# Optimization experiments

Hardware: AMD Instinct MI355X
Metric: run time of the kernel (lower is better)

Reference implementation:

```python
import jax, jax.numpy as jnp
import numpy as np

D_MODEL = 384
N_LAYER = 4
VOCAB = 5000
D_INNER = 768   # 2 * d_model (mamba expand=2)
D_STATE = 16
DT_RANK = 24    # ceil(d_model/16)
D_CONV = 4
EPS = 1e-5
BATCH = 4
SEQ = 2048


def setup_inputs():
    key = jax.random.key(0)
    ks = jax.random.split(key, 12)
    tokens = jax.random.randint(ks[0], (BATCH, SEQ), 0, VOCAB)
    embed = jax.random.normal(ks[1], (VOCAB, D_MODEL), jnp.float32) * 0.02
    norm_w = jnp.ones((N_LAYER, D_MODEL), jnp.float32)
    in_proj_w = jax.random.normal(ks[2], (N_LAYER, 2 * D_INNER, D_MODEL), jnp.float32) * 0.02
    conv_w = jax.random.normal(ks[3], (N_LAYER, D_INNER, D_CONV), jnp.float32) * 0.2
    conv_b = jnp.zeros((N_LAYER, D_INNER), jnp.float32)
    x_proj_w = jax.random.normal(ks[4], (N_LAYER, DT_RANK + 2 * D_STATE, D_INNER), jnp.float32) * 0.05
    dt_proj_w = jax.random.normal(ks[5], (N_LAYER, D_INNER, DT_RANK), jnp.float32) * 0.05
    # bias ~ inverse-softplus of small dt init (dt ~ [0.001, 0.1])
    dt_proj_b = -4.0 + jax.random.normal(ks[6], (N_LAYER, D_INNER), jnp.float32) * 0.5
    # S4D-real init: A = -[1..d_state]
    A_log = jnp.log(jnp.broadcast_to(jnp.arange(1, D_STATE + 1, dtype=jnp.float32), (N_LAYER, D_INNER, D_STATE)))
    D_param = jnp.ones((N_LAYER, D_INNER), jnp.float32)
    out_proj_w = jax.random.normal(ks[7], (N_LAYER, D_MODEL, D_INNER), jnp.float32) * 0.02
    final_norm_w = jnp.ones((D_MODEL,), jnp.float32)
    return {"tokens": tokens, "embed": embed, "norm_w": norm_w, "in_proj_w": in_proj_w,
            "conv_w": conv_w, "conv_b": conv_b, "x_proj_w": x_proj_w, "dt_proj_w": dt_proj_w,
            "dt_proj_b": dt_proj_b, "A_log": A_log, "D_param": D_param,
            "out_proj_w": out_proj_w, "final_norm_w": final_norm_w}


def rmsnorm(x, w):
    return x * w * jax.lax.rsqrt(jnp.mean(x * x, axis=-1, keepdims=True) + EPS)


def mamba_mixer(x, in_w, cw, cb, xpw, dtw, dtb, A_log, Dp, ow):
    B, L, _ = x.shape
    xz = jnp.einsum('bld,ed->ble', x, in_w)          # (B,L,2E)
    xin, z = jnp.split(xz, 2, axis=-1)               # (B,L,E) each
    # causal depthwise conv1d (kernel 4, left-pad 3)
    xc = jnp.swapaxes(xin, 1, 2)                     # (B,E,L)
    xc = jax.lax.conv_general_dilated(
        xc, cw[:, None, :], (1,), [(D_CONV - 1, 0)],
        dimension_numbers=('NCH', 'OIH', 'NCH'), feature_group_count=D_INNER)
    xin = jax.nn.silu(jnp.swapaxes(xc, 1, 2) + cb)   # (B,L,E)
    proj = jnp.einsum('ble,re->blr', xin, xpw)       # (B,L,dtR+2N)
    dt, Bs, Cs = jnp.split(proj, [DT_RANK, DT_RANK + D_STATE], axis=-1)
    dt = jax.nn.softplus(jnp.einsum('blr,er->ble', dt, dtw) + dtb)  # (B,L,E)
    A = -jnp.exp(A_log)                               # (E,N)

    def step(h, inp):
        dt_t, B_t, C_t, x_t = inp                     # (B,E),(B,N),(B,N),(B,E)
        h = h * jnp.exp(dt_t[..., None] * A) + (dt_t * x_t)[..., None] * B_t[:, None, :]
        y = jnp.einsum('ben,bn->be', h, C_t)
        return h, y

    h0 = jnp.zeros((B, D_INNER, D_STATE), x.dtype)
    _, ys = jax.lax.scan(step, h0, (jnp.swapaxes(dt, 0, 1), jnp.swapaxes(Bs, 0, 1),
                                    jnp.swapaxes(Cs, 0, 1), jnp.swapaxes(xin, 0, 1)))
    y = jnp.swapaxes(ys, 0, 1) + xin * Dp             # skip via D
    y = y * jax.nn.silu(z)                            # gate
    return jnp.einsum('ble,de->bld', y, ow)


def reference(tokens, embed, norm_w, in_proj_w, conv_w, conv_b, x_proj_w,
              dt_proj_w, dt_proj_b, A_log, D_param, out_proj_w, final_norm_w):
    x = embed[tokens]                                 # (B,L,D)
    for i in range(N_LAYER):
        x = x + mamba_mixer(rmsnorm(x, norm_w[i]), in_proj_w[i], conv_w[i], conv_b[i],
                            x_proj_w[i], dt_proj_w[i], dt_proj_b[i], A_log[i],
                            D_param[i], out_proj_w[i])
    x = rmsnorm(x, final_norm_w)
    return jnp.einsum('bld,vd->blv', x, embed)        # tied lm_head -> logits
```

## Files before the change

### kernel.cpp

```cpp
#include <hip/hip_runtime.h>
#include <hip/hip_bf16.h>

#define D_MODEL 384
#define N_LAYER 4
#define VOCAB   5000
#define D_INNER 768
#define D_STATE 16
#define DT_RANK 24
#define D_CONV  4
#define BATCH   4
#define SEQ     2048
#define ROWS    (BATCH*SEQ)
#define NCHUNK  64
#define CLEN    32

typedef __attribute__((ext_vector_type(8))) short bf16x8;
typedef __attribute__((ext_vector_type(4))) float f32x4;

static __device__ __forceinline__ ushort f2b(float f) {
    uint u = __float_as_uint(f);
    return (ushort)((u + 0x7FFFu + ((u >> 16) & 1u)) >> 16);
}
static __device__ __forceinline__ float b2f(ushort u) {
    return __uint_as_float((uint)u << 16);
}
static __device__ __forceinline__ float softplus_f(float v) {
    return fmaxf(v, 0.f) + __logf(1.f + __expf(-fabsf(v)));
}

static __device__ __forceinline__ void gl_lds16(const void* g, void* l) {
    __builtin_amdgcn_global_load_lds(
        (const __attribute__((address_space(1))) void*)g,
        (__attribute__((address_space(3))) void*)l, 16, 0, 0);
}

template<int N> static __device__ __forceinline__ void waitcnt_vm() {
    __builtin_amdgcn_s_waitcnt((N & 0xF) | (7 << 4) | (0xF << 8) | (((N >> 4) & 3) << 14));
}

__global__ __launch_bounds__(256)
void prep_k(const float* __restrict__ inw, const float* __restrict__ outw,
            const float* __restrict__ emb, const float* __restrict__ xpw,
            const float* __restrict__ dtw, const int* __restrict__ tokens,
            ushort* __restrict__ inw_b, ushort* __restrict__ outw_b,
            ushort* __restrict__ emb_b, ushort* __restrict__ wf,
            float* __restrict__ x)
{
    int idx = blockIdx.x * 256 + threadIdx.x;
    if (idx < 589824) {
        float4 v = reinterpret_cast<const float4*>(inw)[idx];
        ushort4 o; o.x=f2b(v.x); o.y=f2b(v.y); o.z=f2b(v.z); o.w=f2b(v.w);
        reinterpret_cast<ushort4*>(inw_b)[idx] = o;
    } else if (idx < 884736) {
        int i = idx - 589824;
        float4 v = reinterpret_cast<const float4*>(outw)[i];
        ushort4 o; o.x=f2b(v.x); o.y=f2b(v.y); o.z=f2b(v.z); o.w=f2b(v.w);
        reinterpret_cast<ushort4*>(outw_b)[i] = o;
    } else if (idx < 1364736) {
        int i = idx - 884736;
        float4 v = reinterpret_cast<const float4*>(emb)[i];
        ushort4 o; o.x=f2b(v.x); o.y=f2b(v.y); o.z=f2b(v.z); o.w=f2b(v.w);
        reinterpret_cast<ushort4*>(emb_b)[i] = o;
    } else if (idx < 4117248) {
        int i = idx - 1364736;
        int l = i / (896*768); int rk = i % (896*768);
        int r = rk / 768, k = rk % 768;
        float v = 0.f;
        if (r < 768) {
            const float* dr = dtw + ((size_t)l*768 + r)*24;
            const float* xc = xpw + (size_t)l*56*768 + k;
            #pragma unroll
            for (int q = 0; q < 24; ++q) v += dr[q] * xc[(size_t)q*768];
        } else if (r < 800) {
            v = xpw[((size_t)l*56 + 24 + (r-768))*768 + k];
        }
        wf[i] = f2b(v);
    } else {
        int i = idx - 4117248;
        int row = i / 96, c4 = i % 96;
        int tok = tokens[row];
        reinterpret_cast<float4*>(x)[(size_t)row * 96 + c4] =
            reinterpret_cast<const float4*>(emb)[(size_t)tok * 96 + c4];
    }
}

__global__ __launch_bounds__(256)
void rmsnorm_k(const float* __restrict__ xin, const float* __restrict__ w,
               ushort* __restrict__ xout)
{
    int row  = blockIdx.x * 4 + (threadIdx.x >> 6);
    int lane = threadIdx.x & 63;
    const float* xr = xin + (size_t)row * D_MODEL;
    float v[6]; float ss = 0.f;
    #pragma unroll
    for (int j = 0; j < 6; ++j) { v[j] = xr[lane + 64*j]; ss += v[j]*v[j]; }
    #pragma unroll
    for (int m = 32; m; m >>= 1) ss += __shfl_xor(ss, m, 64);
    float r = rsqrtf(ss * (1.f/D_MODEL) + 1e-5f);
    ushort* yo = xout + (size_t)row * D_MODEL;
    #pragma unroll
    for (int j = 0; j < 6; ++j) yo[lane + 64*j] = f2b(v[j] * w[lane + 64*j] * r);
}

__global__ __launch_bounds__(256)
void conv_silu_k(const ushort* __restrict__ xz_b, const float* __restrict__ cw,
                 const float* __restrict__ cb, ushort* __restrict__ xout_b)
{
    int idx = blockIdx.x * 256 + threadIdx.x;
    int e4  = idx % 192;
    int row = idx / 192;
    int e   = e4 * 4;
    int l   = row & (SEQ - 1);

    float4 w0 = reinterpret_cast<const float4*>(cw)[e4*4 + 0];
    float4 w1 = reinterpret_cast<const float4*>(cw)[e4*4 + 1];
    float4 w2 = reinterpret_cast<const float4*>(cw)[e4*4 + 2];
    float4 w3 = reinterpret_cast<const float4*>(cw)[e4*4 + 3];
    float4 bv = reinterpret_cast<const float4*>(cb)[e4];
    float ac0 = bv.x, ac1 = bv.y, ac2 = bv.z, ac3 = bv.w;

    #pragma unroll
    for (int j = 0; j < 4; ++j) {
        if (l - j >= 0) {
            ushort4 v = *reinterpret_cast<const ushort4*>(
                &xz_b[(size_t)(row - j) * (2*D_INNER) + e]);
            float wj0 = (&w0.x)[3-j], wj1 = (&w1.x)[3-j],
                  wj2 = (&w2.x)[3-j], wj3 = (&w3.x)[3-j];
            ac0 += wj0 * b2f(v.x); ac1 += wj1 * b2f(v.y);
            ac2 += wj2 * b2f(v.z); ac3 += wj3 * b2f(v.w);
        }
    }
    ushort4 o;
    o.x = f2b(ac0 / (1.f + __expf(-ac0)));
    o.y = f2b(ac1 / (1.f + __expf(-ac1)));
    o.z = f2b(ac2 / (1.f + __expf(-ac2)));
    o.w = f2b(ac3 / (1.f + __expf(-ac3)));
    *reinterpret_cast<ushort4*>(&xout_b[(size_t)row * D_INNER + e]) = o;
}

template<int TM, int TN, int EPI>
__global__ __launch_bounds__(256)
void gemm_lds(const ushort* __restrict__ A, int lda,
              const ushort* __restrict__ B, int ldb,
              float* __restrict__ C, int ldc,
              ushort* __restrict__ Cb, const float* __restrict__ bias,
              int N, int K)
{
    constexpr int FM = TM / 32, FN = TN / 32;
    constexpr int LPT = TM/64 + TN/64;
    __shared__ alignas(16) ushort As[3][TM * 32];
    __shared__ alignas(16) ushort Bs[3][TN * 32];
    int tid = threadIdx.x, w = tid >> 6, l = tid & 63;
    int wr = w >> 1, wc = w & 1;
    int row0 = blockIdx.y * TM, col0 = blockIdx.x * TN;
    int l15 = l & 15, g = l >> 4;
    int sr = l >> 2, sp = l & 3;

    f32x4 acc[FM][FN] = {};

    auto stage = [&](int buf, int k0) {
        #pragma unroll
        for (int j = 0; j < TM/64; ++j) {
            int ai = w * (TM/64) + j;
            int r  = ai * 16 + sr;
            int s  = sp ^ ((r >> 1) & 3);
            gl_lds16(&A[(size_t)(row0 + r) * lda + k0 + s*8], &As[buf][ai * 512]);
        }
        #pragma unroll
        for (int j = 0; j < TN/64; ++j) {
            int bi = w * (TN/64) + j;
            int r  = bi * 16 + sr;
            int s  = sp ^ ((r >> 1) & 3);
            gl_lds16(&B[(size_t)(col0 + r) * ldb + k0 + s*8], &Bs[buf][bi * 512]);
        }
    };

    int nk = K >> 5;
    stage(0, 0);
    if (nk > 1) stage(1, 32);

    int cur = 0, sbuf = 2;
    for (int t = 0; t < nk; ++t) {
        if (t < nk - 1) waitcnt_vm<LPT>();
        else            waitcnt_vm<0>();
        __builtin_amdgcn_sched_barrier(0);
        __builtin_amdgcn_s_barrier();
        __builtin_amdgcn_sched_barrier(0);
        if (t + 2 < nk) stage(sbuf, (t + 2) << 5);
        __builtin_amdgcn_sched_barrier(0);

        bf16x8 af[FM], bfr[FN];
        #pragma unroll
        for (int i = 0; i < FM; ++i) {
            int r = wr * (TM/2) + i*16 + l15;
            int p = g ^ ((r >> 1) & 3);
            af[i] = *reinterpret_cast<const bf16x8*>(&As[cur][r*32 + p*8]);
        }
        #pragma unroll
        for (int i = 0; i < FN; ++i) {
            int r = wc * (TN/2) + i*16 + l15;
            int p = g ^ ((r >> 1) & 3);
            bfr[i] = *reinterpret_cast<const bf16x8*>(&Bs[cur][r*32 + p*8]);
        }
        #pragma unroll
        for (int i = 0; i < FM; ++i)
            #pragma unroll
            for (int jj = 0; jj < FN; ++jj)
                acc[i][jj] = __builtin_amdgcn_mfma_f32_16x16x32_bf16(bfr[jj], af[i], acc[i][jj], 0, 0, 0);

        cur  = (cur  == 2) ? 0 : cur + 1;
        sbuf = (sbuf == 2) ? 0 : sbuf + 1;
    }

    #pragma unroll
    for (int i = 0; i < FM; ++i) {
        int m = row0 + wr * (TM/2) + i*16 + l15;
        #pragma unroll
        for (int jj = 0; jj < FN; ++jj) {
            int n0 = col0 + wc * (TN/2) + jj*16 + g*4;
            if (n0 < N) {
                f32x4 v = acc[i][jj];
                if (EPI == 2) {
                    float4* p = reinterpret_cast<float4*>(&C[(size_t)m * ldc + n0]);
                    float4 o = *p;
                    o.x += v[0]; o.y += v[1]; o.z += v[2]; o.w += v[3];
                    *p = o;
                } else if (EPI == 4) {
                    ushort4 o;
                    o.x = f2b(v[0]); o.y = f2b(v[1]); o.z = f2b(v[2]); o.w = f2b(v[3]);
                    *reinterpret_cast<ushort4*>(&Cb[(size_t)m * ldc + n0]) = o;
                } else if (EPI == 5) {
                    if (n0 < 768) {
                        float4 bv = *reinterpret_cast<const float4*>(&bias[n0]);
                        ushort4 o;
                        o.x = f2b(softplus_f(v[0] + bv.x));
                        o.y = f2b(softplus_f(v[1] + bv.y));
                        o.z = f2b(softplus_f(v[2] + bv.z));
                        o.w = f2b(softplus_f(v[3] + bv.w));
                        *reinterpret_cast<ushort4*>(&Cb[(size_t)m * ldc + n0]) = o;
                    } else {
                        float4 o; o.x = v[0]; o.y = v[1]; o.z = v[2]; o.w = v[3];
                        *reinterpret_cast<float4*>(&C[(size_t)m * 32 + (n0 - 768)]) = o;
                    }
                } else {
                    float4 o; o.x = v[0]; o.y = v[1]; o.z = v[2]; o.w = v[3];
                    *reinterpret_cast<float4*>(&C[(size_t)m * ldc + n0]) = o;
                }
            }
        }
    }
}


__global__ __launch_bounds__(256)
void scan_p1(const ushort* __restrict__ dtb, const ushort* __restrict__ xin_b,
             const float* __restrict__ bc, const float* __restrict__ A_log,
             ushort* __restrict__ h_end, ushort* __restrict__ decay)
{
    __shared__ float Bs[CLEN][16];
    int b = blockIdx.z, c = blockIdx.y;
    int e = blockIdx.x * 256 + threadIdx.x;
    size_t r0 = (size_t)b * SEQ + (size_t)c * CLEN;

    for (int i = threadIdx.x; i < CLEN*16; i += 256) {
        int l = i >> 4, n = i & 15;
        Bs[l][n] = bc[(r0 + l) * 32 + n];
    }
    __syncthreads();

    float a[16];
    const float4* ap = reinterpret_cast<const float4*>(A_log + e * D_STATE);
    #pragma unroll
    for (int q = 0; q < 4; ++q) {
        float4 av = ap[q];
        a[q*4+0] = -__expf(av.x); a[q*4+1] = -__expf(av.y);
        a[q*4+2] = -__expf(av.z); a[q*4+3] = -__expf(av.w);
    }

    const ushort* pdt = dtb   + r0 * D_INNER + e;
    const ushort* px  = xin_b + r0 * D_INNER + e;
    float h[16];
    #pragma unroll
    for (int n = 0; n < 16; ++n) h[n] = 0.f;
    float S = 0.f;
    float dtv = b2f(pdt[0]), xv = b2f(px[0]);

    for (int l = 0; l < CLEN; ++l) {
        float dtn = 0.f, xn2 = 0.f;
        if (l + 1 < CLEN) {
            dtn = b2f(pdt[(size_t)(l+1) * D_INNER]);
            xn2 = b2f(px [(size_t)(l+1) * D_INNER]);
        }
        float dtx = dtv * xv;
        S += dtv;
        const float4* br = reinterpret_cast<const float4*>(&Bs[l][0]);
        float4 B0 = br[0], B1 = br[1], B2 = br[2], B3 = br[3];
        float Bv[16] = {B0.x,B0.y,B0.z,B0.w, B1.x,B1.y,B1.z,B1.w,
                        B2.x,B2.y,B2.z,B2.w, B3.x,B3.y,B3.z,B3.w};
        #pragma unroll
        for (int n = 0; n < 16; ++n) {
            float ex = __expf(dtv * a[n]);
            h[n] = h[n] * ex + dtx * Bv[n];
        }
        dtv = dtn; xv = xn2;
    }

    size_t base = (((size_t)b * D_INNER + e) * D_STATE) * NCHUNK + c;
    #pragma unroll
    for (int n = 0; n < 16; ++n) {
        h_end[base + (size_t)n * NCHUNK] = f2b(h[n]);
        decay[base + (size_t)n * NCHUNK] = f2b(__expf(a[n] * S));
    }
}

__global__ __launch_bounds__(256)
void scan_p2(const ushort* __restrict__ h_end, const ushort* __restrict__ decay,
             ushort* __restrict__ h_init)
{
    int wid  = (blockIdx.x * 256 + threadIdx.x) >> 6;
    int lane = threadIdx.x & 63;
    size_t base = (size_t)wid * NCHUNK;
    float d = b2f(decay[base + lane]);
    float v = b2f(h_end[base + lane]);
    #pragma unroll
    for (int off = 1; off < 64; off <<= 1) {
        float dp = __shfl_up(d, off, 64);
        float vp = __shfl_up(v, off, 64);
        if (lane >= off) { v = fmaf(d, vp, v); d *= dp; }
    }
    float hi = __shfl_up(v, 1, 64);
    if (lane == 0) hi = 0.f;
    h_init[base + lane] = f2b(hi);
}

__global__ __launch_bounds__(256)
void scan_p3(const ushort* __restrict__ dtb, const ushort* __restrict__ xin_b,
             const ushort* __restrict__ xz_b, const float* __restrict__ bc,
             const float* __restrict__ A_log, const float* __restrict__ Dp,
             const ushort* __restrict__ h_init, ushort* __restrict__ y)
{
    __shared__ float BCs[CLEN][32];
    int b = blockIdx.z, c = blockIdx.y;
    int e = blockIdx.x * 256 + threadIdx.x;
    size_t r0 = (size_t)b * SEQ + (size_t)c * CLEN;

    for (int i = threadIdx.x; i < CLEN*32; i += 256) {
        int l = i >> 5, r = i & 31;
        BCs[l][r] = bc[(r0 + l) * 32 + r];
    }
    __syncthreads();

    float a[16];
    const float4* ap = reinterpret_cast<const float4*>(A_log + e * D_STATE);
    #pragma unroll
    for (int q = 0; q < 4; ++q) {
        float4 av = ap[q];
        a[q*4+0] = -__expf(av.x); a[q*4+1] = -__expf(av.y);
        a[q*4+2] = -__expf(av.z); a[q*4+3] = -__expf(av.w);
    }
    float dskip = Dp[e];

    float h[16];
    size_t hbase = (((size_t)b * D_INNER + e) * D_STATE) * NCHUNK + c;
    #pragma unroll
    for (int n = 0; n < 16; ++n) h[n] = b2f(h_init[hbase + (size_t)n * NCHUNK]);

    const ushort* pdt = dtb   + r0 * D_INNER + e;
    const ushort* px  = xin_b + r0 * D_INNER + e;
    const ushort* pz  = xz_b  + r0 * (2*D_INNER) + D_INNER + e;
    ushort*       py  = y     + r0 * D_INNER + e;

    float dtv = b2f(pdt[0]), xv = b2f(px[0]), zv = b2f(pz[0]);

    for (int l = 0; l < CLEN; ++l) {
        float dtn = 0.f, xn2 = 0.f, zn = 0.f;
        if (l + 1 < CLEN) {
            dtn = b2f(pdt[(size_t)(l+1) * D_INNER]);
            xn2 = b2f(px [(size_t)(l+1) * D_INNER]);
            zn  = b2f(pz [(size_t)(l+1) * (2*D_INNER)]);
        }
        float dtx = dtv * xv;
        const float4* br = reinterpret_cast<const float4*>(&BCs[l][0]);
        float4 B0 = br[0], B1 = br[1], B2 = br[2], B3 = br[3];
        float Bv[16] = {B0.x,B0.y,B0.z,B0.w, B1.x,B1.y,B1.z,B1.w,
                        B2.x,B2.y,B2.z,B2.w, B3.x,B3.y,B3.z,B3.w};
        #pragma unroll
        for (int n = 0; n < 16; ++n) {
            float ex = __expf(dtv * a[n]);
            h[n] = h[n] * ex + dtx * Bv[n];
        }
        float4 C0 = br[4], C1 = br[5], C2 = br[6], C3 = br[7];
        float Cv[16] = {C0.x,C0.y,C0.z,C0.w, C1.x,C1.y,C1.z,C1.w,
                        C2.x,C2.y,C2.z,C2.w, C3.x,C3.y,C3.z,C3.w};
        float yv = 0.f;
        #pragma unroll
        for (int n = 0; n < 16; ++n) yv += h[n] * Cv[n];

        float g = zv / (1.f + __expf(-zv));
        py[(size_t)l * D_INNER] = f2b((yv + xv * dskip) * g);

        dtv = dtn; xv = xn2; zv = zn;
    }
}

extern "C" void kernel_launch(void* const* d_in, const int* in_sizes, int n_in,
                              void* d_out, int out_size, void* d_ws, size_t ws_size,
                              hipStream_t stream)
{
    const int*   tokens       = (const int*)  d_in[0];
    const float* embed        = (const float*)d_in[1];
    const float* norm_w       = (const float*)d_in[2];
    const float* in_proj_w    = (const float*)d_in[3];
    const float* conv_w       = (const float*)d_in[4];
    const float* conv_b       = (const float*)d_in[5];
    const float* x_proj_w     = (const float*)d_in[6];
    const float* dt_proj_w    = (const float*)d_in[7];
    const float* dt_proj_b    = (const float*)d_in[8];
    const float* A_log        = (const float*)d_in[9];
    const float* D_param      = (const float*)d_in[10];
    const float* out_proj_w   = (const float*)d_in[11];
    const float* final_norm_w = (const float*)d_in[12];
    float* out = (float*)d_out;

    float* ws = (float*)d_ws;
    float*  x      = ws;
    ushort* inw_b  = (ushort*)(ws + 3145728);
    ushort* outw_b = (ushort*)(ws + 4325376);
    ushort* emb_b  = (ushort*)(ws + 4915200);
    ushort* wf_b   = (ushort*)(ws + 5898240);
    float*  bc     = ws + 7274496;
    ushort* xn_b   = (ushort*)(ws + 7536640);

    ushort* xz_b   = (ushort*)out;
    ushort* dtb    = (ushort*)(out + 6291456);
    ushort* y_b    = (ushort*)(out + 9437184);
    ushort* xin_b  = (ushort*)(out + 12582912);
    ushort* h_end  = (ushort*)(out + 15728640);
    ushort* decay  = (ushort*)(out + 17301504);
    ushort* h_init = (ushort*)(out + 18874368);

    dim3 blk(256);

    prep_k<<<19155, blk, 0, stream>>>(in_proj_w, out_proj_w, embed, x_proj_w,
                                      dt_proj_w, tokens,
                                      inw_b, outw_b, emb_b, wf_b, x);

    for (int i = 0; i < N_LAYER; ++i) {
        rmsnorm_k<<<ROWS/4, blk, 0, stream>>>(x, norm_w + i*D_MODEL, xn_b);
        gemm_lds<128,128,4><<<dim3(12, 64), blk, 0, stream>>>(
            xn_b, D_MODEL, inw_b + (size_t)i*2*D_INNER*D_MODEL, D_MODEL,
            nullptr, 2*D_INNER, xz_b, nullptr, 2*D_INNER, D_MODEL);
        conv_silu_k<<<ROWS*192/256, blk, 0, stream>>>(
            xz_b, conv_w + i*D_INNER*D_CONV, conv_b + i*D_INNER, xin_b);
        gemm_lds<128,64,5><<<dim3(13, 64), blk, 0, stream>>>(
            xin_b, D_INNER, wf_b + (size_t)i*896*D_INNER, D_INNER,
            bc, D_INNER, dtb, dt_proj_b + i*D_INNER, 800, D_INNER);
        scan_p1<<<dim3(3, NCHUNK, BATCH), blk, 0, stream>>>(
            dtb, xin_b, bc, A_log + (size_t)i*D_INNER*D_STATE, h_end, decay);
        scan_p2<<<BATCH*D_INNER*D_STATE/4, blk, 0, stream>>>(h_end, decay, h_init);
        scan_p3<<<dim3(3, NCHUNK, BATCH), blk, 0, stream>>>(
            dtb, xin_b, xz_b, bc, A_log + (size_t)i*D_INNER*D_STATE,
            D_param + i*D_INNER, h_init, y_b);
        gemm_lds<64,64,2><<<dim3(6, 128), blk, 0, stream>>>(
            y_b, D_INNER, outw_b + (size_t)i*D_MODEL*D_INNER, D_INNER,
            x, D_MODEL, nullptr, nullptr, D_MODEL, D_INNER);
    }

    rmsnorm_k<<<ROWS/4, blk, 0, stream>>>(x, final_norm_w, xn_b);
    gemm_lds<128,128,0><<<dim3(40, 64), blk, 0, stream>>>(
        xn_b, D_MODEL, emb_b, D_MODEL, out, VOCAB, nullptr, nullptr, VOCAB, D_MODEL);
}
```

Baseline: 933.7 us.

## Fuse three chunked-scan kernels into one cooperative kernel with grid syncs

Merges the chunk-local scan, the cross-chunk prefix combine and the output pass into a single cooperative launch separated by grid-wide barriers. B/C are staged into shared memory once and A is computed once, instead of being reloaded per kernel. This removes two launches per layer and some redundant loads. In exchange it adds two grid syncs, and it requires all 768 blocks to be co-resident, which constrains occupancy; if they cannot all be resident the cooperative launch will fail. The middle phase assigns each wave 16 prefix scans, which covers the required 49152 scans.

```diff
diff --git a/kernel.cpp b/kernel.cpp
--- a/kernel.cpp
+++ b/kernel.cpp
@@ -1,5 +1,8 @@
 #include <hip/hip_runtime.h>
 #include <hip/hip_bf16.h>
+#include <hip/hip_cooperative_groups.h>
+
+namespace cg = cooperative_groups;
 
 #define D_MODEL 384
 #define N_LAYER 4
@@ -251,20 +254,21 @@
     }
 }
 
-
 __global__ __launch_bounds__(256)
-void scan_p1(const ushort* __restrict__ dtb, const ushort* __restrict__ xin_b,
-             const float* __restrict__ bc, const float* __restrict__ A_log,
-             ushort* __restrict__ h_end, ushort* __restrict__ decay)
-{
-    __shared__ float Bs[CLEN][16];
+void scan_fused(const ushort* __restrict__ dtb, const ushort* __restrict__ xin_b,
+                const ushort* __restrict__ xz_b, const float* __restrict__ bc,
+                const float* __restrict__ A_log, const float* __restrict__ Dp,
+                ushort* __restrict__ h_end, ushort* __restrict__ decay,
+                ushort* __restrict__ h_init, ushort* __restrict__ y)
+{
+    __shared__ float BCs[CLEN][32];
     int b = blockIdx.z, c = blockIdx.y;
     int e = blockIdx.x * 256 + threadIdx.x;
     size_t r0 = (size_t)b * SEQ + (size_t)c * CLEN;
 
-    for (int i = threadIdx.x; i < CLEN*16; i += 256) {
-        int l = i >> 4, n = i & 15;
-        Bs[l][n] = bc[(r0 + l) * 32 + n];
+    for (int i = threadIdx.x; i < CLEN*32; i += 256) {
+        int l = i >> 5, r = i & 31;
+        BCs[l][r] = bc[(r0 + l) * 32 + r];
     }
     __syncthreads();
 
@@ -279,127 +283,105 @@
 
     const ushort* pdt = dtb   + r0 * D_INNER + e;
     const ushort* px  = xin_b + r0 * D_INNER + e;
-    float h[16];
-    #pragma unroll
-    for (int n = 0; n < 16; ++n) h[n] = 0.f;
-    float S = 0.f;
-    float dtv = b2f(pdt[0]), xv = b2f(px[0]);
-
-    for (int l = 0; l < CLEN; ++l) {
-        float dtn = 0.f, xn2 = 0.f;
-        if (l + 1 < CLEN) {
-            dtn = b2f(pdt[(size_t)(l+1) * D_INNER]);
-            xn2 = b2f(px [(size_t)(l+1) * D_INNER]);
-        }
-        float dtx = dtv * xv;
-        S += dtv;
-        const float4* br = reinterpret_cast<const float4*>(&Bs[l][0]);
-        float4 B0 = br[0], B1 = br[1], B2 = br[2], B3 = br[3];
-        float Bv[16] = {B0.x,B0.y,B0.z,B0.w, B1.x,B1.y,B1.z,B1.w,
-                        B2.x,B2.y,B2.z,B2.w, B3.x,B3.y,B3.z,B3.w};
+
+    {
+        float h[16];
+        #pragma unroll
+        for (int n = 0; n < 16; ++n) h[n] = 0.f;
+        float S = 0.f;
+        float dtv = b2f(pdt[0]), xv = b2f(px[0]);
+        for (int l = 0; l < CLEN; ++l) {
+            float dtn = 0.f, xn2 = 0.f;
+            if (l + 1 < CLEN) {
+                dtn = b2f(pdt[(size_t)(l+1) * D_INNER]);
+                xn2 = b2f(px [(size_t)(l+1) * D_INNER]);
+            }
+            float dtx = dtv * xv;
+            S += dtv;
+            const float4* br = reinterpret_cast<const float4*>(&BCs[l][0]);
+            float4 B0 = br[0], B1 = br[1], B2 = br[2], B3 = br[3];
+            float Bv[16] = {B0.x,B0.y,B0.z,B0.w, B1.x,B1.y,B1.z,B1.w,
+                            B2.x,B2.y,B2.z,B2.w, B3.x,B3.y,B3.z,B3.w};
+            #pragma unroll
+            for (int n = 0; n < 16; ++n) {
+                float ex = __expf(dtv * a[n]);
+                h[n] = h[n] * ex + dtx * Bv[n];
+            }
+            dtv = dtn; xv = xn2;
+        }
+        size_t base = (((size_t)b * D_INNER + e) * D_STATE) * NCHUNK + c;
         #pragma unroll
         for (int n = 0; n < 16; ++n) {
-            float ex = __expf(dtv * a[n]);
-            h[n] = h[n] * ex + dtx * Bv[n];
-        }
-        dtv = dtn; xv = xn2;
-    }
-
-    size_t base = (((size_t)b * D_INNER + e) * D_STATE) * NCHUNK + c;
-    #pragma unroll
-    for (int n = 0; n < 16; ++n) {
-        h_end[base + (size_t)n * NCHUNK] = f2b(h[n]);
-        decay[base + (size_t)n * NCHUNK] = f2b(__expf(a[n] * S));
-    }
-}
-
-__global__ __launch_bounds__(256)
-void scan_p2(const ushort* __restrict__ h_end, const ushort* __restrict__ decay,
-             ushort* __restrict__ h_init)
-{
-    int wid  = (blockIdx.x * 256 + threadIdx.x) >> 6;
-    int lane = threadIdx.x & 63;
-    size_t base = (size_t)wid * NCHUNK;
-    float d = b2f(decay[base + lane]);
-    float v = b2f(h_end[base + lane]);
-    #pragma unroll
-    for (int off = 1; off < 64; off <<= 1) {
-        float dp = __shfl_up(d, off, 64);
-        float vp = __shfl_up(v, off, 64);
-        if (lane >= off) { v = fmaf(d, vp, v); d *= dp; }
-    }
-    float hi = __shfl_up(v, 1, 64);
-    if (lane == 0) hi = 0.f;
-    h_init[base + lane] = f2b(hi);
-}
-
-__global__ __launch_bounds__(256)
-void scan_p3(const ushort* __restrict__ dtb, const ushort* __restrict__ xin_b,
-             const ushort* __restrict__ xz_b, const float* __restrict__ bc,
-             const float* __restrict__ A_log, const float* __restrict__ Dp,
-             const ushort* __restrict__ h_init, ushort* __restrict__ y)
-{
-    __shared__ float BCs[CLEN][32];
-    int b = blockIdx.z, c = blockIdx.y;
-    int e = blockIdx.x * 256 + threadIdx.x;
-    size_t r0 = (size_t)b * SEQ + (size_t)c * CLEN;
-
-    for (int i = threadIdx.x; i < CLEN*32; i += 256) {
-        int l = i >> 5, r = i & 31;
-        BCs[l][r] = bc[(r0 + l) * 32 + r];
-    }
-    __syncthreads();
-
-    float a[16];
-    const float4* ap = reinterpret_cast<const float4*>(A_log + e * D_STATE);
-    #pragma unroll
-    for (int q = 0; q < 4; ++q) {
-        float4 av = ap[q];
-        a[q*4+0] = -__expf(av.x); a[q*4+1] = -__expf(av.y);
-        a[q*4+2] = -__expf(av.z); a[q*4+3] = -__expf(av.w);
-    }
-    float dskip = Dp[e];
-
-    float h[16];
-    size_t hbase = (((size_t)b * D_INNER + e) * D_STATE) * NCHUNK + c;
-    #pragma unroll
-    for (int n = 0; n < 16; ++n) h[n] = b2f(h_init[hbase + (size_t)n * NCHUNK]);
-
-    const ushort* pdt = dtb   + r0 * D_INNER + e;
-    const ushort* px  = xin_b + r0 * D_INNER + e;
-    const ushort* pz  = xz_b  + r0 * (2*D_INNER) + D_INNER + e;
-    ushort*       py  = y     + r0 * D_INNER + e;
-
-    float dtv = b2f(pdt[0]), xv = b2f(px[0]), zv = b2f(pz[0]);
-
-    for (int l = 0; l < CLEN; ++l) {
-        float dtn = 0.f, xn2 = 0.f, zn = 0.f;
-        if (l + 1 < CLEN) {
-            dtn = b2f(pdt[(size_t)(l+1) * D_INNER]);
-            xn2 = b2f(px [(size_t)(l+1) * D_INNER]);
-            zn  = b2f(pz [(size_t)(l+1) * (2*D_INNER)]);
-        }
-        float dtx = dtv * xv;
-        const float4* br = reinterpret_cast<const float4*>(&BCs[l][0]);
-        float4 B0 = br[0], B1 = br[1], B2 = br[2], B3 = br[3];
-        float Bv[16] = {B0.x,B0.y,B0.z,B0.w, B1.x,B1.y,B1.z,B1.w,
-                        B2.x,B2.y,B2.z,B2.w, B3.x,B3.y,B3.z,B3.w};
-        #pragma unroll
-        for (int n = 0; n < 16; ++n) {
-            float ex = __expf(dtv * a[n]);
-            h[n] = h[n] * ex + dtx * Bv[n];
-        }
-        float4 C0 = br[4], C1 = br[5], C2 = br[6], C3 = br[7];
-        float Cv[16] = {C0.x,C0.y,C0.z,C0.w, C1.x,C1.y,C1.z,C1.w,
-                        C2.x,C2.y,C2.z,C2.w, C3.x,C3.y,C3.z,C3.w};
-        float yv = 0.f;
-        #pragma unroll
-        for (int n = 0; n < 16; ++n) yv += h[n] * Cv[n];
-
-        float g = zv / (1.f + __expf(-zv));
-        py[(size_t)l * D_INNER] = f2b((yv + xv * dskip) * g);
-
-        dtv = dtn; xv = xn2; zv = zn;
+            h_end[base + (size_t)n * NCHUNK] = f2b(h[n]);
+            decay[base + (size_t)n * NCHUNK] = f2b(__expf(a[n] * S));
+        }
+    }
+
+    cg::this_grid().sync();
+
+    {
+        int flatb = blockIdx.x + gridDim.x * (blockIdx.y + gridDim.y * blockIdx.z);
+        int gw    = flatb * 4 + (threadIdx.x >> 6);
+        int lane  = threadIdx.x & 63;
+        #pragma unroll 4
+        for (int t = 0; t < 16; ++t) {
+            size_t base = ((size_t)gw * 16 + t) * NCHUNK;
+            float d = b2f(decay[base + lane]);
+            float v = b2f(h_end[base + lane]);
+            #pragma unroll
+            for (int off = 1; off < 64; off <<= 1) {
+                float dp = __shfl_up(d, off, 64);
+                float vp = __shfl_up(v, off, 64);
+                if (lane >= off) { v = fmaf(d, vp, v); d *= dp; }
+            }
+            float hi = __shfl_up(v, 1, 64);
+            if (lane == 0) hi = 0.f;
+            h_init[base + lane] = f2b(hi);
+        }
+    }
+
+    cg::this_grid().sync();
+
+    {
+        float dskip = Dp[e];
+        float h[16];
+        size_t hbase = (((size_t)b * D_INNER + e) * D_STATE) * NCHUNK + c;
+        #pragma unroll
+        for (int n = 0; n < 16; ++n) h[n] = b2f(h_init[hbase + (size_t)n * NCHUNK]);
+
+        const ushort* pz = xz_b + r0 * (2*D_INNER) + D_INNER + e;
+        ushort*       py = y    + r0 * D_INNER + e;
+
+        float dtv = b2f(pdt[0]), xv = b2f(px[0]), zv = b2f(pz[0]);
+        for (int l = 0; l < CLEN; ++l) {
+            float dtn = 0.f, xn2 = 0.f, zn = 0.f;
+            if (l + 1 < CLEN) {
+                dtn = b2f(pdt[(size_t)(l+1) * D_INNER]);
+                xn2 = b2f(px [(size_t)(l+1) * D_INNER]);
+                zn  = b2f(pz [(size_t)(l+1) * (2*D_INNER)]);
+            }
+            float dtx = dtv * xv;
+            const float4* br = reinterpret_cast<const float4*>(&BCs[l][0]);
+            float4 B0 = br[0], B1 = br[1], B2 = br[2], B3 = br[3];
+            float Bv[16] = {B0.x,B0.y,B0.z,B0.w, B1.x,B1.y,B1.z,B1.w,
+                            B2.x,B2.y,B2.z,B2.w, B3.x,B3.y,B3.z,B3.w};
+            #pragma unroll
+            for (int n = 0; n < 16; ++n) {
+                float ex = __expf(dtv * a[n]);
+                h[n] = h[n] * ex + dtx * Bv[n];
+            }
+            float4 C0 = br[4], C1 = br[5], C2 = br[6], C3 = br[7];
+            float Cv[16] = {C0.x,C0.y,C0.z,C0.w, C1.x,C1.y,C1.z,C1.w,
+                            C2.x,C2.y,C2.z,C2.w, C3.x,C3.y,C3.z,C3.w};
+            float yv = 0.f;
+            #pragma unroll
+            for (int n = 0; n < 16; ++n) yv += h[n] * Cv[n];
+
+            float g = zv / (1.f + __expf(-zv));
+            py[(size_t)l * D_INNER] = f2b((yv + xv * dskip) * g);
+
+            dtv = dtn; xv = xn2; zv = zn;
+        }
     }
 }
 
@@ -455,12 +437,21 @@
         gemm_lds<128,64,5><<<dim3(13, 64), blk, 0, stream>>>(
             xin_b, D_INNER, wf_b + (size_t)i*896*D_INNER, D_INNER,
             bc, D_INNER, dtb, dt_proj_b + i*D_INNER, 800, D_INNER);
-        scan_p1<<<dim3(3, NCHUNK, BATCH), blk, 0, stream>>>(
-            dtb, xin_b, bc, A_log + (size_t)i*D_INNER*D_STATE, h_end, decay);
-        scan_p2<<<BATCH*D_INNER*D_STATE/4, blk, 0, stream>>>(h_end, decay, h_init);
-        scan_p3<<<dim3(3, NCHUNK, BATCH), blk, 0, stream>>>(
-            dtb, xin_b, xz_b, bc, A_log + (size_t)i*D_INNER*D_STATE,
-            D_param + i*D_INNER, h_init, y_b);
+        {
+            const ushort* dtb_c  = dtb;
+            const ushort* xin_c  = xin_b;
+            const ushort* xz_c   = xz_b;
+            const float*  bc_c   = bc;
+            const float*  Al_c   = A_log + (size_t)i*D_INNER*D_STATE;
+            const float*  Dp_c   = D_param + (size_t)i*D_INNER;
+            ushort* he_c = h_end; ushort* de_c = decay; ushort* hi_c = h_init;
+            ushort* y_c  = y_b;
+            void* args[] = { (void*)&dtb_c, (void*)&xin_c, (void*)&xz_c, (void*)&bc_c,
+                             (void*)&Al_c, (void*)&Dp_c, (void*)&he_c, (void*)&de_c,
+                             (void*)&hi_c, (void*)&y_c };
+            hipLaunchCooperativeKernel((const void*)scan_fused,
+                                       dim3(3, NCHUNK, BATCH), blk, args, 0, stream);
+        }
         gemm_lds<64,64,2><<<dim3(6, 128), blk, 0, stream>>>(
             y_b, D_INNER, outw_b + (size_t)i*D_MODEL*D_INNER, D_INNER,
             x, D_MODEL, nullptr, nullptr, D_MODEL, D_INNER);
```

Result: slower. 1.788 ms (+91.5%).

## Fold chunk-carry prefix scan into scan_p3 and drop scan_p2 kernel

Applied to the files above, without the earlier changes.

Removes the separate scan_p2 kernel, which did a shuffle-based prefix over chunk end states. Each scan_p3 thread now rebuilds its initial state by sequentially combining the h_end and decay values of all earlier chunks. The h_end/decay layout changes to state-contiguous per chunk, so both phases use vectorized 16-byte loads and stores. This saves one launch per layer and the h_init round trip. In exchange it adds redundant work that grows with chunk index (up to 63 sequential steps for the last chunk), which causes load imbalance across blocks.

```diff
diff --git a/kernel.cpp b/kernel.cpp
--- a/kernel.cpp
+++ b/kernel.cpp
@@ -305,39 +305,28 @@
         dtv = dtn; xv = xn2;
     }
 
-    size_t base = (((size_t)b * D_INNER + e) * D_STATE) * NCHUNK + c;
-    #pragma unroll
-    for (int n = 0; n < 16; ++n) {
-        h_end[base + (size_t)n * NCHUNK] = f2b(h[n]);
-        decay[base + (size_t)n * NCHUNK] = f2b(__expf(a[n] * S));
-    }
-}
-
-__global__ __launch_bounds__(256)
-void scan_p2(const ushort* __restrict__ h_end, const ushort* __restrict__ decay,
-             ushort* __restrict__ h_init)
-{
-    int wid  = (blockIdx.x * 256 + threadIdx.x) >> 6;
-    int lane = threadIdx.x & 63;
-    size_t base = (size_t)wid * NCHUNK;
-    float d = b2f(decay[base + lane]);
-    float v = b2f(h_end[base + lane]);
-    #pragma unroll
-    for (int off = 1; off < 64; off <<= 1) {
-        float dp = __shfl_up(d, off, 64);
-        float vp = __shfl_up(v, off, 64);
-        if (lane >= off) { v = fmaf(d, vp, v); d *= dp; }
-    }
-    float hi = __shfl_up(v, 1, 64);
-    if (lane == 0) hi = 0.f;
-    h_init[base + lane] = f2b(hi);
+    size_t base = ((((size_t)b * D_INNER + e) * NCHUNK) + c) * 16;
+    bf16x8 hv0, hv1, dv0, dv1;
+    float dcy[16];
+    #pragma unroll
+    for (int n = 0; n < 16; ++n) dcy[n] = __expf(a[n] * S);
+    #pragma unroll
+    for (int n = 0; n < 8; ++n) {
+        hv0[n] = (short)f2b(h[n]);     hv1[n] = (short)f2b(h[8+n]);
+        dv0[n] = (short)f2b(dcy[n]);   dv1[n] = (short)f2b(dcy[8+n]);
+    }
+    *reinterpret_cast<bf16x8*>(&h_end[base])     = hv0;
+    *reinterpret_cast<bf16x8*>(&h_end[base + 8]) = hv1;
+    *reinterpret_cast<bf16x8*>(&decay[base])     = dv0;
+    *reinterpret_cast<bf16x8*>(&decay[base + 8]) = dv1;
 }
 
 __global__ __launch_bounds__(256)
 void scan_p3(const ushort* __restrict__ dtb, const ushort* __restrict__ xin_b,
              const ushort* __restrict__ xz_b, const float* __restrict__ bc,
              const float* __restrict__ A_log, const float* __restrict__ Dp,
-             const ushort* __restrict__ h_init, ushort* __restrict__ y)
+             const ushort* __restrict__ h_end, const ushort* __restrict__ decay,
+             ushort* __restrict__ y)
 {
     __shared__ float BCs[CLEN][32];
     int b = blockIdx.z, c = blockIdx.y;
@@ -348,6 +337,26 @@
         int l = i >> 5, r = i & 31;
         BCs[l][r] = bc[(r0 + l) * 32 + r];
     }
+
+    float h[16];
+    #pragma unroll
+    for (int n = 0; n < 16; ++n) h[n] = 0.f;
+    {
+        size_t sbase = (((size_t)b * D_INNER + e) * NCHUNK) * 16;
+        const ushort* he = h_end + sbase;
+        const ushort* de = decay + sbase;
+        for (int cc = 0; cc < c; ++cc) {
+            bf16x8 hv0 = *reinterpret_cast<const bf16x8*>(he + cc*16);
+            bf16x8 hv1 = *reinterpret_cast<const bf16x8*>(he + cc*16 + 8);
+            bf16x8 dv0 = *reinterpret_cast<const bf16x8*>(de + cc*16);
+            bf16x8 dv1 = *reinterpret_cast<const bf16x8*>(de + cc*16 + 8);
+            #pragma unroll
+            for (int n = 0; n < 8; ++n) {
+                h[n]   = fmaf(b2f((ushort)dv0[n]), h[n],   b2f((ushort)hv0[n]));
+                h[8+n] = fmaf(b2f((ushort)dv1[n]), h[8+n], b2f((ushort)hv1[n]));
+            }
+        }
+    }
     __syncthreads();
 
     float a[16];
@@ -359,11 +368,6 @@
         a[q*4+2] = -__expf(av.z); a[q*4+3] = -__expf(av.w);
     }
     float dskip = Dp[e];
-
-    float h[16];
-    size_t hbase = (((size_t)b * D_INNER + e) * D_STATE) * NCHUNK + c;
-    #pragma unroll
-    for (int n = 0; n < 16; ++n) h[n] = b2f(h_init[hbase + (size_t)n * NCHUNK]);
 
     const ushort* pdt = dtb   + r0 * D_INNER + e;
     const ushort* px  = xin_b + r0 * D_INNER + e;
@@ -437,7 +441,6 @@
     ushort* xin_b  = (ushort*)(out + 12582912);
     ushort* h_end  = (ushort*)(out + 15728640);
     ushort* decay  = (ushort*)(out + 17301504);
-    ushort* h_init = (ushort*)(out + 18874368);
 
     dim3 blk(256);
 
@@ -457,10 +460,9 @@
             bc, D_INNER, dtb, dt_proj_b + i*D_INNER, 800, D_INNER);
         scan_p1<<<dim3(3, NCHUNK, BATCH), blk, 0, stream>>>(
             dtb, xin_b, bc, A_log + (size_t)i*D_INNER*D_STATE, h_end, decay);
-        scan_p2<<<BATCH*D_INNER*D_STATE/4, blk, 0, stream>>>(h_end, decay, h_init);
         scan_p3<<<dim3(3, NCHUNK, BATCH), blk, 0, stream>>>(
             dtb, xin_b, xz_b, bc, A_log + (size_t)i*D_INNER*D_STATE,
-            D_param + i*D_INNER, h_init, y_b);
+            D_param + i*D_INNER, h_end, decay, y_b);
         gemm_lds<64,64,2><<<dim3(6, 128), blk, 0, stream>>>(
             y_b, D_INNER, outw_b + (size_t)i*D_MODEL*D_INNER, D_INNER,
             x, D_MODEL, nullptr, nullptr, D_MODEL, D_INNER);
```

New measurement: 952.4 us. 2.0% more time.
